# Performance work log

Measured on AMD Instinct MI355X. Metric: run time of the kernel, lower is better.

The kernel has to match this reference:

```python
import jax, jax.numpy as jnp
import numpy as np


def setup_inputs() -> dict:
    key = jax.random.key(0)
    k1, k2, k3, k4 = jax.random.split(key, 4)
    B, Q, D, H = 8, 512, 4096, 1024
    return {
        "query_embeddings": jax.random.normal(k1, (B, Q, H), dtype=jnp.float32),
        "document_embeddings": jax.random.normal(k2, (B, D, H), dtype=jnp.float32),
        "attention_mask": jax.random.randint(k3, (B, D), 0, 2, dtype=jnp.int32),
        "proj_w": jax.random.normal(k4, (H, H), dtype=jnp.float32) * (H ** -0.5),
        "proj_b": jnp.zeros((H,), dtype=jnp.float32),
    }


def reference(query_embeddings, document_embeddings, attention_mask, proj_w, proj_b):
    H = query_embeddings.shape[-1]
    scale = 1.0 / jnp.sqrt(jnp.asarray(H, dtype=query_embeddings.dtype))
    # Linear projection of queries: [B, Q, H]
    q = jnp.einsum("bqh,hk->bqk", query_embeddings, proj_w) + proj_b
    # Scores: [B, Q, D]
    scores = jnp.einsum("bqh,bdh->bqd", q, document_embeddings) * scale
    # Mask: [B, 1, D]; masked positions -> -inf before softmax
    mask = attention_mask[:, None, :] != 0
    scores = jnp.where(mask, scores, -jnp.inf)
    attention_weights = jax.nn.softmax(scores, axis=-1)
    # Weighted sum over docs: [B, Q, H]
    retrieved_docs = jnp.einsum("bqd,bdh->bqh", attention_weights, document_embeddings)
    return (retrieved_docs, attention_weights)
```

## Files before the change

### kernel.cpp

```cpp
#include <hip/hip_runtime.h>

#define BATCH 8
#define QLEN 512
#define DLEN 4096
#define HDIM 1024

typedef __attribute__((ext_vector_type(8))) short bf16x8;
typedef __attribute__((ext_vector_type(4))) float f32x4;
typedef __attribute__((ext_vector_type(4))) short s16x4;

__device__ __forceinline__ short f2bf(float f) {
    union { float f; unsigned u; } x; x.f = f;
    unsigned r = x.u + 0x7fffu + ((x.u >> 16) & 1u);
    return (short)(r >> 16);
}

__device__ __forceinline__ void gload_lds16(const void* g, void* l) {
    __builtin_amdgcn_global_load_lds(
        (const __attribute__((address_space(1))) unsigned int*)g,
        (__attribute__((address_space(3))) unsigned int*)l,
        16, 0, 0);
}

#define WAIT_VMCNT(n) asm volatile("s_waitcnt vmcnt(" #n ")" ::: "memory")

__global__ void cvt_f32_bf16(const float* __restrict__ in, short* __restrict__ out, int n4) {
    int i = blockIdx.x * blockDim.x + threadIdx.x;
    int stride = gridDim.x * blockDim.x;
    for (; i < n4; i += stride) {
        float4 x = ((const float4*)in)[i];
        s16x4 o = { f2bf(x.x), f2bf(x.y), f2bf(x.z), f2bf(x.w) };
        ((s16x4*)out)[i] = o;
    }
}

__global__ void transpose_w(const float* __restrict__ W, short* __restrict__ Wt) {
    __shared__ float t[32][33];
    const int hb = blockIdx.y * 32, kb = blockIdx.x * 32;
    #pragma unroll
    for (int i = 0; i < 4; ++i) {
        int h = threadIdx.y + i * 8;
        t[h][threadIdx.x] = W[(size_t)(hb + h) * HDIM + kb + threadIdx.x];
    }
    __syncthreads();
    #pragma unroll
    for (int i = 0; i < 4; ++i) {
        int k = threadIdx.y + i * 8;
        Wt[(size_t)(kb + k) * HDIM + hb + threadIdx.x] = f2bf(t[threadIdx.x][k]);
    }
}

__global__ void transpose_docs(const short* __restrict__ docsB, short* __restrict__ docsT) {
    __shared__ unsigned t[64][65];
    const int b = blockIdx.z;
    const int h0 = blockIdx.x * 64, d0 = blockIdx.y * 64;
    const int tq = threadIdx.x & 15;
    const int tr = threadIdx.x >> 4;
    #pragma unroll
    for (int i = 0; i < 4; ++i) {
        int d = tr + i * 16;
        s16x4 v = *(const s16x4*)(docsB + ((size_t)b * DLEN + d0 + d) * HDIM + h0 + tq * 4);
        t[d][tq * 4 + 0] = (unsigned short)v[0];
        t[d][tq * 4 + 1] = (unsigned short)v[1];
        t[d][tq * 4 + 2] = (unsigned short)v[2];
        t[d][tq * 4 + 3] = (unsigned short)v[3];
    }
    __syncthreads();
    #pragma unroll
    for (int i = 0; i < 4; ++i) {
        int h = tr + i * 16;
        s16x4 o = { (short)t[tq * 4 + 0][h], (short)t[tq * 4 + 1][h],
                    (short)t[tq * 4 + 2][h], (short)t[tq * 4 + 3][h] };
        *(s16x4*)(docsT + ((size_t)b * HDIM + h0 + h) * DLEN + d0 + tq * 4) = o;
    }
}

#define BM 128
#define BN 128
#define BK 32
#define TILE_SH (BM * BK)

template<int EPI>
__global__ void gemm_bt(const short* __restrict__ A, const short* __restrict__ B,
                        void* __restrict__ Cv, const float* __restrict__ bias,
                        float scale, int N, int Kstride, int Kloop, int kOffStep,
                        int sx, int sxy,
                        long long aB, long long bB, long long cB) {
    __shared__ short As[3 * TILE_SH];
    __shared__ short Bs[3 * TILE_SH];
    const int tid  = threadIdx.x;
    const int lane = tid & 63;
    const int wv   = tid >> 6;
    const int wr   = wv >> 1, wc = wv & 1;

    const int wg = (blockIdx.x & 7) * (gridDim.x >> 3) + (blockIdx.x >> 3);
    const int bx = wg & ((1 << sx) - 1);
    const int by = (wg >> sx) & ((1 << (sxy - sx)) - 1);
    const int z  = wg >> sxy;

    const size_t rowBase = (size_t)by * BM;
    const size_t colBase = (size_t)bx * BN;
    const int bb = z & 7;
    const int kOff = (z >> 3) * kOffStep;
    const short* Ag = A + (size_t)bb * aB + kOff;
    const short* Bg = B + (size_t)bb * bB + kOff;

    f32x4 acc[4][4];
    #pragma unroll
    for (int m = 0; m < 4; ++m)
        #pragma unroll
        for (int n = 0; n < 4; ++n)
            acc[m][n] = (f32x4){0.f, 0.f, 0.f, 0.f};

    const short* aSrc[2]; const short* bSrc[2]; int dOff[2];
    #pragma unroll
    for (int i = 0; i < 2; ++i) {
        const int c = tid + 256 * i;
        const int r = c >> 2, cc = c & 3;
        const int gk = (cc ^ ((r >> 1) & 3)) << 3;
        aSrc[i] = Ag + (rowBase + r) * (size_t)Kstride + gk;
        bSrc[i] = Bg + (colBase + r) * (size_t)Kstride + gk;
        dOff[i] = c * 8;
    }
    const int chunkL = lane >> 4;
    const int lr = lane & 15;

    const int nt = Kloop / BK;

    #pragma unroll
    for (int i = 0; i < 2; ++i) gload_lds16(aSrc[i], As + dOff[i]);
    #pragma unroll
    for (int i = 0; i < 2; ++i) gload_lds16(bSrc[i], Bs + dOff[i]);
    #pragma unroll
    for (int i = 0; i < 2; ++i) gload_lds16(aSrc[i] + BK, As + TILE_SH + dOff[i]);
    #pragma unroll
    for (int i = 0; i < 2; ++i) gload_lds16(bSrc[i] + BK, Bs + TILE_SH + dOff[i]);
    WAIT_VMCNT(4);
    __builtin_amdgcn_s_barrier();

    for (int t = 0; t < nt; ++t) {
        if (t + 2 < nt) {
            const int kt = (t + 2) * BK;
            const int o = ((t + 2) % 3) * TILE_SH;
            #pragma unroll
            for (int i = 0; i < 2; ++i) gload_lds16(aSrc[i] + kt, As + o + dOff[i]);
            #pragma unroll
            for (int i = 0; i < 2; ++i) gload_lds16(bSrc[i] + kt, Bs + o + dOff[i]);
        }

        const short* Ab = As + (t % 3) * TILE_SH;
        const short* Bb = Bs + (t % 3) * TILE_SH;
        bf16x8 af[4], bfr[4];
        #pragma unroll
        for (int m = 0; m < 4; ++m) {
            const int row = wr * 64 + m * 16 + lr;
            af[m] = *(const bf16x8*)(Ab + row * BK + ((chunkL ^ ((row >> 1) & 3)) << 3));
        }
        #pragma unroll
        for (int n = 0; n < 4; ++n) {
            const int row = wc * 64 + n * 16 + lr;
            bfr[n] = *(const bf16x8*)(Bb + row * BK + ((chunkL ^ ((row >> 1) & 3)) << 3));
        }
        #pragma unroll
        for (int m = 0; m < 4; ++m)
            #pragma unroll
            for (int n = 0; n < 4; ++n)
                acc[m][n] = __builtin_amdgcn_mfma_f32_16x16x32_bf16(af[m], bfr[n], acc[m][n], 0, 0, 0);

        if (t + 1 < nt) {
            if (t + 2 < nt) { WAIT_VMCNT(4); }
            else           { WAIT_VMCNT(0); }
            __builtin_amdgcn_sched_barrier(0);
            __builtin_amdgcn_s_barrier();
            __builtin_amdgcn_sched_barrier(0);
        }
    }

    const int orow = (lane >> 4) << 2;
    const int ocol = lane & 15;
    #pragma unroll
    for (int n = 0; n < 4; ++n) {
        const size_t col = colBase + wc * 64 + n * 16 + ocol;
        const float bv = (EPI == 0) ? bias[col] : 0.f;
        #pragma unroll
        for (int m = 0; m < 4; ++m) {
            const size_t rbase = rowBase + wr * 64 + m * 16 + orow;
            #pragma unroll
            for (int j = 0; j < 4; ++j) {
                const float v = acc[m][n][j];
                const size_t off = (size_t)z * cB + (rbase + j) * (size_t)N + col;
                if (EPI == 0)      ((short*)Cv)[off] = f2bf(v + bv);
                else if (EPI == 1) ((float*)Cv)[off] = v * scale;
                else               ((float*)Cv)[off] = v;
            }
        }
    }
}

__global__ void reduce4(const float* __restrict__ p, float* __restrict__ out, int n4) {
    int i = blockIdx.x * blockDim.x + threadIdx.x;
    const int stride = gridDim.x * blockDim.x;
    const float4* p4 = (const float4*)p;
    float4* o4 = (float4*)out;
    for (; i < n4; i += stride) {
        float4 a = p4[i];
        float4 b = p4[i + 1048576];
        float4 c = p4[i + 2097152];
        float4 d = p4[i + 3145728];
        float4 r;
        r.x = a.x + b.x + c.x + d.x;
        r.y = a.y + b.y + c.y + d.y;
        r.z = a.z + b.z + c.z + d.z;
        r.w = a.w + b.w + c.w + d.w;
        o4[i] = r;
    }
}

__global__ void softmax_rows(const float* __restrict__ scores, const int* __restrict__ mask,
                             float* __restrict__ attnF, short* __restrict__ attnB) {
    const int row = blockIdx.x;
    const int b   = row >> 9;
    const int tid = threadIdx.x;
    const int lane = tid & 63;
    const int wv = tid >> 6;
    const float4* S  = (const float4*)(scores + (size_t)row * DLEN);
    const int4*   Mk = (const int4*)(mask + (size_t)b * DLEN);
    __shared__ float red[8];

    float v[16];
    float mx = -INFINITY;
    #pragma unroll
    for (int i = 0; i < 4; ++i) {
        float4 s = S[i * 256 + tid];
        int4   m = Mk[i * 256 + tid];
        v[i * 4 + 0] = m.x ? s.x : -INFINITY;
        v[i * 4 + 1] = m.y ? s.y : -INFINITY;
        v[i * 4 + 2] = m.z ? s.z : -INFINITY;
        v[i * 4 + 3] = m.w ? s.w : -INFINITY;
        #pragma unroll
        for (int c = 0; c < 4; ++c) mx = fmaxf(mx, v[i * 4 + c]);
    }
    #pragma unroll
    for (int o = 32; o > 0; o >>= 1) mx = fmaxf(mx, __shfl_xor(mx, o));
    if (lane == 0) red[wv] = mx;
    __syncthreads();
    mx = fmaxf(fmaxf(red[0], red[1]), fmaxf(red[2], red[3]));

    float sum = 0.f;
    #pragma unroll
    for (int i = 0; i < 16; ++i) {
        float e = __expf(v[i] - mx);
        v[i] = e;
        sum += e;
    }
    #pragma unroll
    for (int o = 32; o > 0; o >>= 1) sum += __shfl_xor(sum, o);
    __syncthreads();
    if (lane == 0) red[4 + wv] = sum;
    __syncthreads();
    sum = red[4] + red[5] + red[6] + red[7];
    const float inv = 1.0f / sum;

    float4* OF = (float4*)(attnF + (size_t)row * DLEN);
    s16x4*  OB = (s16x4*)(attnB + (size_t)row * DLEN);
    #pragma unroll
    for (int i = 0; i < 4; ++i) {
        float4 w;
        w.x = v[i * 4 + 0] * inv;
        w.y = v[i * 4 + 1] * inv;
        w.z = v[i * 4 + 2] * inv;
        w.w = v[i * 4 + 3] * inv;
        OF[i * 256 + tid] = w;
        s16x4 o = { f2bf(w.x), f2bf(w.y), f2bf(w.z), f2bf(w.w) };
        OB[i * 256 + tid] = o;
    }
}

extern "C" void kernel_launch(void* const* d_in, const int* in_sizes, int n_in,
                              void* d_out, int out_size, void* d_ws, size_t ws_size,
                              hipStream_t stream) {
    const float* qe   = (const float*)d_in[0];
    const float* docs = (const float*)d_in[1];
    const int*   mask = (const int*)d_in[2];
    const float* pw   = (const float*)d_in[3];
    const float* pb   = (const float*)d_in[4];

    float* outRet  = (float*)d_out;
    float* outAttn = outRet + (size_t)BATCH * QLEN * HDIM;

    char* ws = (char*)d_ws;
    short* qeB   = (short*)(ws + 0);
    short* wt    = (short*)(ws + 8388608);
    short* qpB   = (short*)(ws + 10485760);
    short* docsB = (short*)(ws + 18874368);
    short* docsT = (short*)(ws + 85983232);
    float* scor  = (float*)(ws + 153092096);
    short* attnB = (short*)(ws + 220200960);

    cvt_f32_bf16<<<dim3(1024), dim3(256), 0, stream>>>(qe, qeB, (BATCH * QLEN * HDIM) / 4);
    cvt_f32_bf16<<<dim3(2048), dim3(256), 0, stream>>>(docs, docsB, (BATCH * DLEN * HDIM) / 4);
    transpose_w<<<dim3(32, 32), dim3(32, 8), 0, stream>>>(pw, wt);
    transpose_docs<<<dim3(HDIM / 64, DLEN / 64, BATCH), dim3(256), 0, stream>>>(docsB, docsT);

    gemm_bt<0><<<dim3(256), dim3(256), 0, stream>>>(
        qeB, wt, (void*)qpB, pb, 1.f, HDIM, HDIM, HDIM, 0, 3, 8,
        0LL, 0LL, 0LL);

    gemm_bt<1><<<dim3(1024), dim3(256), 0, stream>>>(
        qpB, docsB, (void*)scor, nullptr, 0.03125f, DLEN, HDIM, HDIM, 0, 5, 7,
        (long long)QLEN * HDIM, (long long)DLEN * HDIM, (long long)QLEN * DLEN);

    softmax_rows<<<dim3(BATCH * QLEN), dim3(256), 0, stream>>>(scor, mask, outAttn, attnB);

    gemm_bt<2><<<dim3(1024), dim3(256), 0, stream>>>(
        attnB, docsT, (void*)scor, nullptr, 1.f, HDIM, DLEN, DLEN / 4, DLEN / 4, 3, 5,
        (long long)QLEN * DLEN, (long long)HDIM * DLEN, (long long)QLEN * HDIM);

    reduce4<<<dim3(2048), dim3(256), 0, stream>>>(scor, outRet, (BATCH * QLEN * HDIM) / 4);
}
```

Measured before the change: 452.3 us.

## Use 256x256 tiles with 512 threads for score and retrieval GEMMs

```diff
diff --git a/kernel.cpp b/kernel.cpp
--- a/kernel.cpp
+++ b/kernel.cpp
@@ -75,19 +75,15 @@
     }
 }
 
-#define BM 128
-#define BN 128
-#define BK 32
-#define TILE_SH (BM * BK)
-
-template<int EPI>
-__global__ void gemm_bt(const short* __restrict__ A, const short* __restrict__ B,
-                        void* __restrict__ Cv, const float* __restrict__ bias,
-                        float scale, int N, int Kstride, int Kloop, int kOffStep,
-                        int sx, int sxy,
-                        long long aB, long long bB, long long cB) {
-    __shared__ short As[3 * TILE_SH];
-    __shared__ short Bs[3 * TILE_SH];
+#define G1BM 128
+#define G1BN 128
+#define G1BK 64
+
+__global__ void gemm128_bias(const short* __restrict__ A, const short* __restrict__ B,
+                             short* __restrict__ C, const float* __restrict__ bias,
+                             int N, int Kstride, int Kloop, int sx, int sxy) {
+    __shared__ short As[G1BM * G1BK];
+    __shared__ short Bs[G1BN * G1BK];
     const int tid  = threadIdx.x;
     const int lane = tid & 63;
     const int wv   = tid >> 6;
@@ -96,18 +92,111 @@
     const int wg = (blockIdx.x & 7) * (gridDim.x >> 3) + (blockIdx.x >> 3);
     const int bx = wg & ((1 << sx) - 1);
     const int by = (wg >> sx) & ((1 << (sxy - sx)) - 1);
+
+    const size_t rowBase = (size_t)by * G1BM;
+    const size_t colBase = (size_t)bx * G1BN;
+
+    f32x4 acc[4][4];
+    #pragma unroll
+    for (int m = 0; m < 4; ++m)
+        #pragma unroll
+        for (int n = 0; n < 4; ++n)
+            acc[m][n] = (f32x4){0.f, 0.f, 0.f, 0.f};
+
+    const short* aSrc[4]; const short* bSrc[4]; int dOff[4];
+    #pragma unroll
+    for (int i = 0; i < 4; ++i) {
+        const int c = tid + 256 * i;
+        const int r = c >> 3, cc = c & 7;
+        const int gk = (cc ^ (r & 7)) << 3;
+        aSrc[i] = A + (rowBase + r) * (size_t)Kstride + gk;
+        bSrc[i] = B + (colBase + r) * (size_t)Kstride + gk;
+        dOff[i] = c * 8;
+    }
+    const int lr = lane & 15;
+    const int lk = (lane >> 4) << 3;
+
+    for (int kt = 0; kt < Kloop; kt += G1BK) {
+        #pragma unroll
+        for (int i = 0; i < 4; ++i) gload_lds16(aSrc[i] + kt, As + dOff[i]);
+        #pragma unroll
+        for (int i = 0; i < 4; ++i) gload_lds16(bSrc[i] + kt, Bs + dOff[i]);
+        __syncthreads();
+
+        #pragma unroll
+        for (int kk = 0; kk < 2; ++kk) {
+            const int chunkL = (kk * 32 + lk) >> 3;
+            bf16x8 af[4], bfr[4];
+            #pragma unroll
+            for (int m = 0; m < 4; ++m) {
+                const int row = wr * 64 + m * 16 + lr;
+                af[m] = *(const bf16x8*)(As + row * G1BK + ((chunkL ^ (row & 7)) << 3));
+            }
+            #pragma unroll
+            for (int n = 0; n < 4; ++n) {
+                const int row = wc * 64 + n * 16 + lr;
+                bfr[n] = *(const bf16x8*)(Bs + row * G1BK + ((chunkL ^ (row & 7)) << 3));
+            }
+            #pragma unroll
+            for (int m = 0; m < 4; ++m)
+                #pragma unroll
+                for (int n = 0; n < 4; ++n)
+                    acc[m][n] = __builtin_amdgcn_mfma_f32_16x16x32_bf16(af[m], bfr[n], acc[m][n], 0, 0, 0);
+        }
+        __syncthreads();
+    }
+
+    const int orow = (lane >> 4) << 2;
+    const int ocol = lane & 15;
+    #pragma unroll
+    for (int n = 0; n < 4; ++n) {
+        const size_t col = colBase + wc * 64 + n * 16 + ocol;
+        const float bv = bias[col];
+        #pragma unroll
+        for (int m = 0; m < 4; ++m) {
+            const size_t rbase = rowBase + wr * 64 + m * 16 + orow;
+            #pragma unroll
+            for (int j = 0; j < 4; ++j)
+                C[(rbase + j) * (size_t)N + col] = f2bf(acc[m][n][j] + bv);
+        }
+    }
+}
+
+#define G2BM 256
+#define G2BN 256
+#define G2BK 32
+#define G2TS (G2BM * G2BK)
+
+template<int EPI>
+__launch_bounds__(512, 1)
+__global__ void gemm256(const short* __restrict__ A, const short* __restrict__ B,
+                        float* __restrict__ Cv, float scale,
+                        int N, int Kstride, int Kloop, int kOffStep,
+                        int sx, int sxy,
+                        long long aB, long long bB, long long cB) {
+    __shared__ short As[3 * G2TS];
+    __shared__ short Bs[3 * G2TS];
+    const int tid  = threadIdx.x;
+    const int lane = tid & 63;
+    const int wv   = tid >> 6;
+    const int wm   = wv >> 2;
+    const int wn   = wv & 3;
+
+    const int wg = (blockIdx.x & 7) * (gridDim.x >> 3) + (blockIdx.x >> 3);
+    const int bx = wg & ((1 << sx) - 1);
+    const int by = (wg >> sx) & ((1 << (sxy - sx)) - 1);
     const int z  = wg >> sxy;
 
-    const size_t rowBase = (size_t)by * BM;
-    const size_t colBase = (size_t)bx * BN;
+    const size_t rowBase = (size_t)by * G2BM;
+    const size_t colBase = (size_t)bx * G2BN;
     const int bb = z & 7;
     const int kOff = (z >> 3) * kOffStep;
     const short* Ag = A + (size_t)bb * aB + kOff;
     const short* Bg = B + (size_t)bb * bB + kOff;
 
-    f32x4 acc[4][4];
-    #pragma unroll
-    for (int m = 0; m < 4; ++m)
+    f32x4 acc[8][4];
+    #pragma unroll
+    for (int m = 0; m < 8; ++m)
         #pragma unroll
         for (int n = 0; n < 4; ++n)
             acc[m][n] = (f32x4){0.f, 0.f, 0.f, 0.f};
@@ -115,7 +204,7 @@
     const short* aSrc[2]; const short* bSrc[2]; int dOff[2];
     #pragma unroll
     for (int i = 0; i < 2; ++i) {
-        const int c = tid + 256 * i;
+        const int c = tid + 512 * i;
         const int r = c >> 2, cc = c & 3;
         const int gk = (cc ^ ((r >> 1) & 3)) << 3;
         aSrc[i] = Ag + (rowBase + r) * (size_t)Kstride + gk;
@@ -125,44 +214,44 @@
     const int chunkL = lane >> 4;
     const int lr = lane & 15;
 
-    const int nt = Kloop / BK;
+    const int nt = Kloop / G2BK;
 
     #pragma unroll
     for (int i = 0; i < 2; ++i) gload_lds16(aSrc[i], As + dOff[i]);
     #pragma unroll
     for (int i = 0; i < 2; ++i) gload_lds16(bSrc[i], Bs + dOff[i]);
     #pragma unroll
-    for (int i = 0; i < 2; ++i) gload_lds16(aSrc[i] + BK, As + TILE_SH + dOff[i]);
-    #pragma unroll
-    for (int i = 0; i < 2; ++i) gload_lds16(bSrc[i] + BK, Bs + TILE_SH + dOff[i]);
+    for (int i = 0; i < 2; ++i) gload_lds16(aSrc[i] + G2BK, As + G2TS + dOff[i]);
+    #pragma unroll
+    for (int i = 0; i < 2; ++i) gload_lds16(bSrc[i] + G2BK, Bs + G2TS + dOff[i]);
     WAIT_VMCNT(4);
     __builtin_amdgcn_s_barrier();
 
     for (int t = 0; t < nt; ++t) {
         if (t + 2 < nt) {
-            const int kt = (t + 2) * BK;
-            const int o = ((t + 2) % 3) * TILE_SH;
+            const int kt = (t + 2) * G2BK;
+            const int o = ((t + 2) % 3) * G2TS;
             #pragma unroll
             for (int i = 0; i < 2; ++i) gload_lds16(aSrc[i] + kt, As + o + dOff[i]);
             #pragma unroll
             for (int i = 0; i < 2; ++i) gload_lds16(bSrc[i] + kt, Bs + o + dOff[i]);
         }
 
-        const short* Ab = As + (t % 3) * TILE_SH;
-        const short* Bb = Bs + (t % 3) * TILE_SH;
-        bf16x8 af[4], bfr[4];
-        #pragma unroll
-        for (int m = 0; m < 4; ++m) {
-            const int row = wr * 64 + m * 16 + lr;
-            af[m] = *(const bf16x8*)(Ab + row * BK + ((chunkL ^ ((row >> 1) & 3)) << 3));
-        }
+        const short* Ab = As + (t % 3) * G2TS;
+        const short* Bb = Bs + (t % 3) * G2TS;
+        bf16x8 bfr[4], af[8];
         #pragma unroll
         for (int n = 0; n < 4; ++n) {
-            const int row = wc * 64 + n * 16 + lr;
-            bfr[n] = *(const bf16x8*)(Bb + row * BK + ((chunkL ^ ((row >> 1) & 3)) << 3));
-        }
-        #pragma unroll
-        for (int m = 0; m < 4; ++m)
+            const int row = wn * 64 + n * 16 + lr;
+            bfr[n] = *(const bf16x8*)(Bb + row * G2BK + ((chunkL ^ ((row >> 1) & 3)) << 3));
+        }
+        #pragma unroll
+        for (int m = 0; m < 8; ++m) {
+            const int row = wm * 128 + m * 16 + lr;
+            af[m] = *(const bf16x8*)(Ab + row * G2BK + ((chunkL ^ ((row >> 1) & 3)) << 3));
+        }
+        #pragma unroll
+        for (int m = 0; m < 8; ++m)
             #pragma unroll
             for (int n = 0; n < 4; ++n)
                 acc[m][n] = __builtin_amdgcn_mfma_f32_16x16x32_bf16(af[m], bfr[n], acc[m][n], 0, 0, 0);
@@ -180,18 +269,15 @@
     const int ocol = lane & 15;
     #pragma unroll
     for (int n = 0; n < 4; ++n) {
-        const size_t col = colBase + wc * 64 + n * 16 + ocol;
-        const float bv = (EPI == 0) ? bias[col] : 0.f;
-        #pragma unroll
-        for (int m = 0; m < 4; ++m) {
-            const size_t rbase = rowBase + wr * 64 + m * 16 + orow;
+        const size_t col = colBase + wn * 64 + n * 16 + ocol;
+        #pragma unroll
+        for (int m = 0; m < 8; ++m) {
+            const size_t rbase = rowBase + wm * 128 + m * 16 + orow;
             #pragma unroll
             for (int j = 0; j < 4; ++j) {
                 const float v = acc[m][n][j];
                 const size_t off = (size_t)z * cB + (rbase + j) * (size_t)N + col;
-                if (EPI == 0)      ((short*)Cv)[off] = f2bf(v + bv);
-                else if (EPI == 1) ((float*)Cv)[off] = v * scale;
-                else               ((float*)Cv)[off] = v;
+                Cv[off] = (EPI == 1) ? v * scale : v;
             }
         }
     }
@@ -302,18 +388,17 @@
     transpose_w<<<dim3(32, 32), dim3(32, 8), 0, stream>>>(pw, wt);
     transpose_docs<<<dim3(HDIM / 64, DLEN / 64, BATCH), dim3(256), 0, stream>>>(docsB, docsT);
 
-    gemm_bt<0><<<dim3(256), dim3(256), 0, stream>>>(
-        qeB, wt, (void*)qpB, pb, 1.f, HDIM, HDIM, HDIM, 0, 3, 8,
-        0LL, 0LL, 0LL);
-
-    gemm_bt<1><<<dim3(1024), dim3(256), 0, stream>>>(
-        qpB, docsB, (void*)scor, nullptr, 0.03125f, DLEN, HDIM, HDIM, 0, 5, 7,
+    gemm128_bias<<<dim3(256), dim3(256), 0, stream>>>(
+        qeB, wt, qpB, pb, HDIM, HDIM, HDIM, 3, 8);
+
+    gemm256<1><<<dim3(256), dim3(512), 0, stream>>>(
+        qpB, docsB, scor, 0.03125f, DLEN, HDIM, HDIM, 0, 4, 5,
         (long long)QLEN * HDIM, (long long)DLEN * HDIM, (long long)QLEN * DLEN);
 
     softmax_rows<<<dim3(BATCH * QLEN), dim3(256), 0, stream>>>(scor, mask, outAttn, attnB);
 
-    gemm_bt<2><<<dim3(1024), dim3(256), 0, stream>>>(
-        attnB, docsT, (void*)scor, nullptr, 1.f, HDIM, DLEN, DLEN / 4, DLEN / 4, 3, 5,
+    gemm256<2><<<dim3(256), dim3(512), 0, stream>>>(
+        attnB, docsT, scor, 1.f, HDIM, DLEN, DLEN / 4, DLEN / 4, 2, 3,
         (long long)QLEN * DLEN, (long long)HDIM * DLEN, (long long)QLEN * HDIM);
 
     reduce4<<<dim3(2048), dim3(256), 0, stream>>>(scor, outRet, (BATCH * QLEN * HDIM) / 4);
```

New measurement: 427.6 us. 5.4% less time.
